# Optimization experiments

Measured on AMD Instinct MI355X. Metric: run time of the kernel, lower is better.

The kernel has to match this reference:

```python
import jax, jax.numpy as jnp
import numpy as np

EPS = 1e-6      # vector-neuron epsilon
BN_EPS = 1e-5   # torch BatchNorm eps
NEG = 0.2       # LeakyReLU negative slope
K = 20


def knn_idx(flat, k):
    # flat: [B, D, N] flattened (C*3) features; returns kNN indices [B, N, k]
    xx = jnp.sum(flat * flat, axis=1)                     # [B, N]
    inner = jnp.einsum('bdn,bdm->bnm', flat, flat)        # [B, N, N]
    neg_dist = 2.0 * inner - xx[:, :, None] - xx[:, None, :]
    return jax.lax.top_k(neg_dist, k)[1]                  # [B, N, k]


def graph_feature(x, k):
    # x: [B, C, 3, N] -> [B, 2C, 3, N, k] = cat(neighbor - center, center)
    B, C, _, N = x.shape
    idx = knn_idx(x.reshape(B, C * 3, N), k)              # [B, N, k]
    xt = jnp.transpose(x, (0, 3, 1, 2))                   # [B, N, C, 3]
    nbr = jax.vmap(lambda f, i: f[i])(xt, idx)            # [B, N, k, C, 3]
    ctr = jnp.broadcast_to(xt[:, :, None], nbr.shape)
    feat = jnp.concatenate([nbr - ctr, ctr], axis=3)      # [B, N, k, 2C, 3]
    return jnp.transpose(feat, (0, 3, 4, 1, 2))


def vn_bn(x, w, b):
    # VNBatchNorm (training-mode batch stats): normalize the per-vector norm.
    # x: [B, C, 3, ...]
    norm = jnp.sqrt(jnp.sum(x * x, axis=2)) + EPS         # [B, C, ...]
    axes = (0,) + tuple(range(2, norm.ndim))
    mean = jnp.mean(norm, axis=axes, keepdims=True)
    var = jnp.mean((norm - mean) ** 2, axis=axes, keepdims=True)
    shp = (1, -1) + (1,) * (norm.ndim - 2)
    nbn = (norm - mean) / jnp.sqrt(var + BN_EPS) * w.reshape(shp) + b.reshape(shp)
    return x * jnp.expand_dims(nbn / norm, 2)


def vn_lrelu(x, wf, wd, bnw, bnb):
    # VNLinearLeakyReLU: linear over channel dim, VN batchnorm, directional LeakyReLU
    p = jnp.einsum('oi,bi...->bo...', wf, x)
    p = vn_bn(p, bnw, bnb)
    d = jnp.einsum('oi,bi...->bo...', wd, x)
    dot = jnp.sum(p * d, axis=2, keepdims=True)
    dsq = jnp.sum(d * d, axis=2, keepdims=True)
    mask = (dot >= 0).astype(x.dtype)
    return NEG * p + (1.0 - NEG) * (mask * p + (1.0 - mask) * (p - (dot / (dsq + EPS)) * d))


def setup_inputs() -> dict:
    key = jax.random.key(0)
    ks = jax.random.split(key, 12)
    H, C = 64, 128
    lin = lambda k, o, i: jax.random.normal(k, (o, i), jnp.float32) / np.sqrt(i)
    return {
        'x': jax.random.normal(ks[0], (8, 1024, 3), jnp.float32),
        'w1f': lin(ks[1], H, 2), 'w1d': lin(ks[2], H, 2),
        'bn1w': jnp.ones(H), 'bn1b': jnp.zeros(H),
        'w2f': lin(ks[3], H, 2 * H), 'w2d': lin(ks[4], H, 2 * H),
        'bn2w': jnp.ones(H), 'bn2b': jnp.zeros(H),
        'w3f': lin(ks[5], H, 2 * H), 'w3d': lin(ks[6], H, 2 * H),
        'bn3w': jnp.ones(H), 'bn3b': jnp.zeros(H),
        'w4f': lin(ks[7], H, 2 * H), 'w4d': lin(ks[8], H, 2 * H),
        'bn4w': jnp.ones(H), 'bn4b': jnp.zeros(H),
        'wcf': lin(ks[9], C, 4 * H), 'wcd': lin(ks[10], 1, 4 * H),
        'bncw': jnp.ones(C), 'bncb': jnp.zeros(C),
    }


def reference(x, w1f, w1d, bn1w, bn1b, w2f, w2d, bn2w, bn2b,
              w3f, w3d, bn3w, bn3b, w4f, w4d, bn4w, bn4b,
              wcf, wcd, bncw, bncb):
    pts = jnp.transpose(x, (0, 2, 1))[:, None]            # [B, 1, 3, N]
    h = vn_lrelu(graph_feature(pts, K), w1f, w1d, bn1w, bn1b)
    x1 = jnp.mean(h, axis=-1)                             # [B, H, 3, N]
    h = vn_lrelu(graph_feature(x1, K), w2f, w2d, bn2w, bn2b)
    x2 = jnp.mean(h, axis=-1)
    h = vn_lrelu(graph_feature(x2, K), w3f, w3d, bn3w, bn3b)
    x3 = jnp.mean(h, axis=-1)
    h = vn_lrelu(graph_feature(x3, K), w4f, w4d, bn4w, bn4b)
    x4 = jnp.mean(h, axis=-1)
    cat = jnp.concatenate([x1, x2, x3, x4], axis=1)       # [B, 4H, 3, N]
    out = vn_lrelu(cat, wcf, wcd, bncw, bncb)             # [B, c_dim, 3, N]
    return jnp.mean(out, axis=-1)                         # [B, c_dim, 3]
```

## Files before the change

kernel.cpp:

```cpp
#include <hip/hip_runtime.h>

#define NPTS 1024
#define NB 8
#define KNN 20
#define N3 (3*NPTS)
#define CHT 256
#define BSX (CHT*N3)

constexpr int OFF_X0    = 0;
constexpr int OFF_XFEAT = OFF_X0 + NB*N3;
constexpr int OFF_YAP   = OFF_XFEAT + NB*CHT*N3;
constexpr int OFF_YBP   = OFF_YAP + NB*N3*64;
constexpr int OFF_YAD   = OFF_YBP + NB*N3*64;
constexpr int OFF_YBD   = OFF_YAD + NB*N3*64;
constexpr int OFF_XX    = OFF_YBD + NB*N3*64;
constexpr int OFF_WCFT  = OFF_XX + NB*NPTS;
constexpr int OFF_STATS = OFF_WCFT + 256*128;
constexpr int OFF_IDX   = OFF_STATS + 5*256;
constexpr int OFF_PF    = OFF_YAP;
constexpr int OFF_DF    = OFF_YAD;

__global__ void k_transpose(const float* __restrict__ x, float* __restrict__ x0) {
  int t = blockIdx.x*256 + threadIdx.x;
  int b = t >> 10, n = t & 1023;
  const float* p = x + t*3;
  x0[b*N3 + n]          = p[0];
  x0[b*N3 + NPTS + n]   = p[1];
  x0[b*N3 + 2*NPTS + n] = p[2];
}

__global__ __launch_bounds__(256) void k_xx2(const float* __restrict__ Fb, int bs, int D,
                                             float* __restrict__ xx) {
  __shared__ float sm[4][64];
  int tid = threadIdx.x;
  int p = tid & 63, g = tid >> 6;
  int t = blockIdx.x * 64 + p;
  int b = t >> 10, m = t & 1023;
  int s = (D * g) >> 2, e = (D * (g + 1)) >> 2;
  const float* f = Fb + b*bs + m;
  float a = 0.f;
  for (int d = s; d < e; ++d) { float v = f[d*NPTS]; a = fmaf(v, v, a); }
  sm[g][p] = a;
  __syncthreads();
  if (g == 0) xx[t] = ((sm[0][p] + sm[1][p]) + sm[2][p]) + sm[3][p];
}

__global__ __launch_bounds__(512) void k_knn2(const float* __restrict__ Fb, int bs, int D,
                                              const float* __restrict__ xx,
                                              int* __restrict__ idxo) {
  __shared__ float xs[8][NPTS];
  int g  = blockIdx.x;
  int wg = (g & 7)*64 + (g >> 3);
  int b  = wg >> 6;
  int n0 = (wg & 63) << 4;
  int tid = threadIdx.x;
  int w = tid >> 6, lane = tid & 63;
  const float* f = Fb + b*bs;

  int row0 = n0 + 2*w, row1 = row0 + 1;
  float acc0[16], acc1[16];
  #pragma unroll
  for (int s = 0; s < 16; ++s) { acc0[s] = 0.f; acc1[s] = 0.f; }

  int nt = (D + 7) >> 3;
  for (int t = 0; t < nt; ++t) {
    int d0 = t << 3;
    int cnt = D - d0; if (cnt > 8) cnt = 8;
    __syncthreads();
    #pragma unroll
    for (int u = 0; u < 4; ++u) {
      int e = tid + (u << 9);
      int dd = e >> 8, mq = (e & 255) << 2;
      if (dd < cnt)
        *(float4*)&xs[dd][mq] = *(const float4*)&f[(d0 + dd)*NPTS + mq];
    }
    __syncthreads();
    for (int dd = 0; dd < cnt; ++dd) {
      float rf0 = xs[dd][row0];
      float rf1 = xs[dd][row1];
      #pragma unroll
      for (int s2 = 0; s2 < 4; ++s2) {
        float4 xm = *(const float4*)&xs[dd][(lane << 2) + (s2 << 8)];
        acc0[s2*4+0] = fmaf(rf0, xm.x, acc0[s2*4+0]);
        acc0[s2*4+1] = fmaf(rf0, xm.y, acc0[s2*4+1]);
        acc0[s2*4+2] = fmaf(rf0, xm.z, acc0[s2*4+2]);
        acc0[s2*4+3] = fmaf(rf0, xm.w, acc0[s2*4+3]);
        acc1[s2*4+0] = fmaf(rf1, xm.x, acc1[s2*4+0]);
        acc1[s2*4+1] = fmaf(rf1, xm.y, acc1[s2*4+1]);
        acc1[s2*4+2] = fmaf(rf1, xm.z, acc1[s2*4+2]);
        acc1[s2*4+3] = fmaf(rf1, xm.w, acc1[s2*4+3]);
      }
    }
  }

  unsigned ord0[16], ord1[16];
  float xxr0 = xx[b*NPTS + row0];
  float xxr1 = xx[b*NPTS + row1];
  #pragma unroll
  for (int s2 = 0; s2 < 4; ++s2) {
    float4 xv = *(const float4*)&xx[b*NPTS + (lane << 2) + (s2 << 8)];
    float xm4[4] = {xv.x, xv.y, xv.z, xv.w};
    #pragma unroll
    for (int q = 0; q < 4; ++q) {
      int s = s2*4 + q;
      float v0 = (2.f*acc0[s] - xxr0) - xm4[q];
      float v1 = (2.f*acc1[s] - xxr1) - xm4[q];
      unsigned u0 = __float_as_uint(v0);
      unsigned u1 = __float_as_uint(v1);
      ord0[s] = (u0 & 0x80000000u) ? ~u0 : (u0 | 0x80000000u);
      ord1[s] = (u1 & 0x80000000u) ? ~u1 : (u1 | 0x80000000u);
    }
  }

  unsigned base4L = (unsigned)(lane << 2);
  unsigned cl0 = 0xFFFFFFFFu, cl1 = 0xFFFFFFFFu;
  int winm0 = 0, winm1 = 0;
  for (int it = 0; it < KNN; ++it) {
    unsigned bo0 = 0u, bc0 = 0u, bo1 = 0u, bc1 = 0u;
    #pragma unroll
    for (int s = 0; s < 16; ++s) {
      const unsigned Cs = (unsigned)(((s >> 2) << 8) | (s & 3));
      unsigned v0 = ord0[s]; v0 = (cl0 == Cs) ? 0u : v0; ord0[s] = v0;
      if (v0 > bo0) { bo0 = v0; bc0 = Cs; }
      unsigned v1 = ord1[s]; v1 = (cl1 == Cs) ? 0u : v1; ord1[s] = v1;
      if (v1 > bo1) { bo1 = v1; bc1 = Cs; }
    }
    unsigned m0 = base4L + bc0, m1 = base4L + bc1;
    unsigned long long K0 = ((unsigned long long)bo0 << 32) | (unsigned long long)(1023u - m0);
    unsigned long long K1 = ((unsigned long long)bo1 << 32) | (unsigned long long)(1023u - m1);
    unsigned long long myK0 = K0, myK1 = K1;
    #pragma unroll
    for (int off = 1; off < 64; off <<= 1) {
      unsigned long long o0 = __shfl_xor(K0, off, 64);
      unsigned long long o1 = __shfl_xor(K1, off, 64);
      K0 = (o0 > K0) ? o0 : K0;
      K1 = (o1 > K1) ? o1 : K1;
    }
    cl0 = (K0 == myK0) ? bc0 : 0xFFFFFFFFu;
    cl1 = (K1 == myK1) ? bc1 : 0xFFFFFFFFu;
    if (lane == it) {
      winm0 = 1023 - (int)(unsigned)(K0 & 0xFFFFFFFFull);
      winm1 = 1023 - (int)(unsigned)(K1 & 0xFFFFFFFFull);
    }
  }
  if (lane < KNN) {
    idxo[(b*NPTS + row0)*KNN + lane] = winm0;
    idxo[(b*NPTS + row1)*KNN + lane] = winm1;
  }
}

template<int DIN>
__global__ __launch_bounds__(256) void k_linear3(const float* __restrict__ xin, int bsx,
                                                 const float* __restrict__ w,
                                                 float* __restrict__ yA, float* __restrict__ yB) {
  __shared__ float wA[DIN*64], wB[DIN*64];
  int tid = threadIdx.x;
  for (int e = tid; e < 64*DIN; e += 256) {
    int o = e & 63, i = e >> 6;
    float a = w[o*(2*DIN) + i];
    wA[i*64 + o] = a;
    wB[i*64 + o] = w[o*(2*DIN) + DIN + i] - a;
  }
  __syncthreads();
  int o = tid & 63, ns = tid >> 6;
  int b = blockIdx.y / 3, v = blockIdx.y % 3;
  int n0 = blockIdx.x * 64 + ns * 16;
  const float* xb = xin + b*bsx + v*NPTS + n0;
  float ap[16], bp[16];
  #pragma unroll
  for (int j = 0; j < 16; ++j) { ap[j] = 0.f; bp[j] = 0.f; }
  for (int i = 0; i < DIN; ++i) {
    float wa = wA[i*64 + o], wb = wB[i*64 + o];
    #pragma unroll
    for (int q = 0; q < 4; ++q) {
      float4 xv = *(const float4*)&xb[i*N3 + q*4];
      ap[q*4+0] = fmaf(wa, xv.x, ap[q*4+0]); bp[q*4+0] = fmaf(wb, xv.x, bp[q*4+0]);
      ap[q*4+1] = fmaf(wa, xv.y, ap[q*4+1]); bp[q*4+1] = fmaf(wb, xv.y, bp[q*4+1]);
      ap[q*4+2] = fmaf(wa, xv.z, ap[q*4+2]); bp[q*4+2] = fmaf(wb, xv.z, bp[q*4+2]);
      ap[q*4+3] = fmaf(wa, xv.w, ap[q*4+3]); bp[q*4+3] = fmaf(wb, xv.w, bp[q*4+3]);
    }
  }
  int base = ((b*3 + v)*NPTS + n0)*64 + o;
  #pragma unroll
  for (int j = 0; j < 16; ++j) { yA[base + j*64] = ap[j]; yB[base + j*64] = bp[j]; }
}

__global__ __launch_bounds__(256) void k_stats2(const float* __restrict__ yAp, const float* __restrict__ yBp,
                                                const int* __restrict__ idxo, float* __restrict__ statsL) {
  __shared__ float rs[256], rss[256];
  int tid = threadIdx.x; int o = tid & 63, w = tid >> 6;
  int blk = blockIdx.x;
  int wg = ((blk & 7) << 8) | (blk >> 3);
  int b = wg >> 8;
  int n = ((wg & 255) << 2) + w;
  float s = 0.f, ss = 0.f;
  int i0 = (b*3*NPTS + n)*64 + o;
  float c0 = yBp[i0], c1 = yBp[i0 + NPTS*64], c2 = yBp[i0 + 2*NPTS*64];
  const int* ir = idxo + (b*NPTS + n)*KNN;
  for (int kk = 0; kk < KNN; ++kk) {
    int m = ir[kk];
    int gg = (b*3*NPTS + m)*64 + o;
    float p0 = yAp[gg] + c0;
    float p1 = yAp[gg + NPTS*64] + c1;
    float p2 = yAp[gg + 2*NPTS*64] + c2;
    float nrm = sqrtf(p0*p0 + p1*p1 + p2*p2) + 1e-6f;
    s += nrm; ss = fmaf(nrm, nrm, ss);
  }
  rs[tid] = s; rss[tid] = ss;
  __syncthreads();
  if (tid < 64) {
    float a  = rs[tid]  + rs[tid+64]  + rs[tid+128]  + rs[tid+192];
    float as = rss[tid] + rss[tid+64] + rss[tid+128] + rss[tid+192];
    atomicAdd(&statsL[tid], a);
    atomicAdd(&statsL[128 + tid], as);
  }
}

__global__ __launch_bounds__(256) void k_apply(const float* __restrict__ yAp, const float* __restrict__ yBp,
                                               const float* __restrict__ yAd, const float* __restrict__ yBd,
                                               const int* __restrict__ idxo, const float* __restrict__ statsL,
                                               const float* __restrict__ bnw, const float* __restrict__ bnb,
                                               float* __restrict__ xfeat, int coff) {
  int tid = threadIdx.x; int o = tid & 63, w = tid >> 6;
  int blk = blockIdx.x;
  int wg = ((blk & 7) << 8) | (blk >> 3);
  int b = wg >> 8;
  int n = ((wg & 255) << 2) + w;
  const float cntInv = 1.f / 163840.f;
  float mean = statsL[o] * cntInv;
  float var  = statsL[128 + o] * cntInv - mean*mean;
  float istd = rsqrtf(var + 1e-5f);
  float wN = bnw[o], bN = bnb[o];
  int i0 = (b*3*NPTS + n)*64 + o;
  float cp0 = yBp[i0], cp1 = yBp[i0 + NPTS*64], cp2 = yBp[i0 + 2*NPTS*64];
  float cd0 = yBd[i0], cd1 = yBd[i0 + NPTS*64], cd2 = yBd[i0 + 2*NPTS*64];
  const int* ir = idxo + (b*NPTS + n)*KNN;
  float a0 = 0.f, a1 = 0.f, a2 = 0.f;
  for (int kk = 0; kk < KNN; ++kk) {
    int m = ir[kk];
    int gg = (b*3*NPTS + m)*64 + o;
    float p0 = yAp[gg] + cp0, p1 = yAp[gg + NPTS*64] + cp1, p2 = yAp[gg + 2*NPTS*64] + cp2;
    float d0 = yAd[gg] + cd0, d1 = yAd[gg + NPTS*64] + cd1, d2 = yAd[gg + 2*NPTS*64] + cd2;
    float nrm = sqrtf(p0*p0 + p1*p1 + p2*p2) + 1e-6f;
    float sc = ((nrm - mean)*istd*wN + bN) / nrm;
    p0 *= sc; p1 *= sc; p2 *= sc;
    float dot = p0*d0 + p1*d1 + p2*d2;
    float dsq = d0*d0 + d1*d1 + d2*d2;
    float coef = (dot < 0.f) ? (0.8f * dot / (dsq + 1e-6f)) : 0.f;
    a0 += p0 - coef*d0; a1 += p1 - coef*d1; a2 += p2 - coef*d2;
  }
  int ob = ((b*CHT + coff + o)*3)*NPTS + n;
  xfeat[ob]          = a0 * 0.05f;
  xfeat[ob + NPTS]   = a1 * 0.05f;
  xfeat[ob + 2*NPTS] = a2 * 0.05f;
}

__global__ void k_wcfT(const float* __restrict__ wcf, float* __restrict__ wT) {
  int e = blockIdx.x*256 + threadIdx.x;
  int o = e >> 8, i = e & 255;
  wT[i*128 + o] = wcf[e];
}

__global__ __launch_bounds__(256) void k_pF3(const float* __restrict__ xfeat, const float* __restrict__ wT,
                                             const float* __restrict__ wcd,
                                             float* __restrict__ pF, float* __restrict__ dF) {
  __shared__ float xs[256][32];
  __shared__ float dpart[8][32];
  int tid = threadIdx.x;
  int b = blockIdx.y / 3, v = blockIdx.y % 3;
  int n0 = blockIdx.x * 32;
  const float* xb = xfeat + b*BSX + v*NPTS + n0;
  #pragma unroll
  for (int u = 0; u < 8; ++u) {
    int e = tid + (u << 8);
    int i = e >> 3, sl = (e & 7) << 2;
    *(float4*)&xs[i][sl] = *(const float4*)&xb[i*N3 + sl];
  }
  __syncthreads();
  int o = tid & 127, h = tid >> 7;
  float a[16];
  #pragma unroll
  for (int j = 0; j < 16; ++j) a[j] = 0.f;
  for (int i = 0; i < 256; ++i) {
    float wv = wT[i*128 + o];
    #pragma unroll
    for (int q = 0; q < 4; ++q) {
      float4 xv = *(const float4*)&xs[i][h*16 + q*4];
      a[q*4+0] = fmaf(wv, xv.x, a[q*4+0]);
      a[q*4+1] = fmaf(wv, xv.y, a[q*4+1]);
      a[q*4+2] = fmaf(wv, xv.z, a[q*4+2]);
      a[q*4+3] = fmaf(wv, xv.w, a[q*4+3]);
    }
  }
  int base = ((b*3 + v)*NPTS + n0 + h*16)*128 + o;
  #pragma unroll
  for (int j = 0; j < 16; ++j) pF[base + j*128] = a[j];
  int nn = tid & 31, gI = tid >> 5;
  float dp = 0.f;
  for (int i = gI*32; i < gI*32 + 32; ++i) dp = fmaf(wcd[i], xs[i][nn], dp);
  dpart[gI][nn] = dp;
  __syncthreads();
  if (tid < 32) {
    float aa = 0.f;
    #pragma unroll
    for (int gq = 0; gq < 8; ++gq) aa += dpart[gq][tid];
    dF[(b*3 + v)*NPTS + n0 + tid] = aa;
  }
}

__global__ __launch_bounds__(256) void k_statsF2(const float* __restrict__ pF, float* __restrict__ statsF) {
  int tid = threadIdx.x; int o = tid & 127, half = tid >> 7;
  int blk = blockIdx.x;
  int b = blk >> 6, n0 = (blk & 63) << 4;
  float s = 0.f, ss = 0.f;
  for (int j = 0; j < 8; ++j) {
    int n = n0 + half + (j << 1);
    int g = (b*3*NPTS + n)*128 + o;
    float p0 = pF[g], p1 = pF[g + NPTS*128], p2 = pF[g + 2*NPTS*128];
    float nrm = sqrtf(p0*p0 + p1*p1 + p2*p2) + 1e-6f;
    s += nrm; ss = fmaf(nrm, nrm, ss);
  }
  atomicAdd(&statsF[o], s);
  atomicAdd(&statsF[128 + o], ss);
}

__global__ __launch_bounds__(256) void k_final2(const float* __restrict__ pF, const float* __restrict__ dF,
                                                const float* __restrict__ statsF,
                                                const float* __restrict__ bncw, const float* __restrict__ bncb,
                                                float* __restrict__ out) {
  int tid = threadIdx.x; int o = tid & 127, half = tid >> 7;
  int blk = blockIdx.x;
  int b = blk >> 5, n0 = (blk & 31) << 5;
  const float cntInv = 1.f / 8192.f;
  float mean = statsF[o] * cntInv;
  float var  = statsF[128 + o] * cntInv - mean*mean;
  float istd = rsqrtf(var + 1e-5f);
  float wN = bncw[o], bN = bncb[o];
  float a0 = 0.f, a1 = 0.f, a2 = 0.f;
  for (int j = 0; j < 16; ++j) {
    int n = n0 + half + (j << 1);
    int g = (b*3*NPTS + n)*128 + o;
    float p0 = pF[g], p1 = pF[g + NPTS*128], p2 = pF[g + 2*NPTS*128];
    int dg = b*N3 + n;
    float d0 = dF[dg], d1 = dF[dg + NPTS], d2 = dF[dg + 2*NPTS];
    float nrm = sqrtf(p0*p0 + p1*p1 + p2*p2) + 1e-6f;
    float sc = ((nrm - mean)*istd*wN + bN) / nrm;
    p0 *= sc; p1 *= sc; p2 *= sc;
    float dot = p0*d0 + p1*d1 + p2*d2;
    float dsq = d0*d0 + d1*d1 + d2*d2;
    float coef = (dot < 0.f) ? (0.8f * dot / (dsq + 1e-6f)) : 0.f;
    a0 += p0 - coef*d0; a1 += p1 - coef*d1; a2 += p2 - coef*d2;
  }
  float scl = 1.f / 1024.f;
  int ob = (b*128 + o)*3;
  atomicAdd(&out[ob],     a0*scl);
  atomicAdd(&out[ob + 1], a1*scl);
  atomicAdd(&out[ob + 2], a2*scl);
}

extern "C" void kernel_launch(void* const* d_in, const int* in_sizes, int n_in,
                              void* d_out, int out_size, void* d_ws, size_t ws_size,
                              hipStream_t stream) {
  (void)in_sizes; (void)n_in; (void)ws_size;
  const float* x = (const float*)d_in[0];
  const float* wF[4]  = {(const float*)d_in[1],  (const float*)d_in[5],
                         (const float*)d_in[9],  (const float*)d_in[13]};
  const float* wD[4]  = {(const float*)d_in[2],  (const float*)d_in[6],
                         (const float*)d_in[10], (const float*)d_in[14]};
  const float* bnW[4] = {(const float*)d_in[3],  (const float*)d_in[7],
                         (const float*)d_in[11], (const float*)d_in[15]};
  const float* bnB[4] = {(const float*)d_in[4],  (const float*)d_in[8],
                         (const float*)d_in[12], (const float*)d_in[16]};
  const float* wcf  = (const float*)d_in[17];
  const float* wcd  = (const float*)d_in[18];
  const float* bncw = (const float*)d_in[19];
  const float* bncb = (const float*)d_in[20];

  float* ws    = (float*)d_ws;
  float* x0    = ws + OFF_X0;
  float* xfeat = ws + OFF_XFEAT;
  float* yAp   = ws + OFF_YAP;
  float* yBp   = ws + OFF_YBP;
  float* yAd   = ws + OFF_YAD;
  float* yBd   = ws + OFF_YBD;
  float* pF    = ws + OFF_PF;
  float* dF    = ws + OFF_DF;
  float* xx    = ws + OFF_XX;
  float* wT    = ws + OFF_WCFT;
  float* stats = ws + OFF_STATS;
  int*   idx   = (int*)(ws + OFF_IDX);

  hipMemsetAsync(stats, 0, 5*256*sizeof(float), stream);
  hipMemsetAsync(d_out, 0, (size_t)out_size*sizeof(float), stream);

  k_transpose<<<NB*NPTS/256, 256, 0, stream>>>(x, x0);
  k_wcfT<<<128, 256, 0, stream>>>(wcf, wT);

  for (int L = 0; L < 4; ++L) {
    const float* fin = (L == 0) ? x0 : (xfeat + (L-1)*64*N3);
    int bs = (L == 0) ? N3 : BSX;
    int D  = (L == 0) ? 3 : 192;
    k_xx2<<<NB*NPTS/64, 256, 0, stream>>>(fin, bs, D, xx);
    k_knn2<<<512, 512, 0, stream>>>(fin, bs, D, xx, idx);
    if (L == 0) {
      k_linear3<1><<<dim3(16, 24), 256, 0, stream>>>(fin, bs, wF[0], yAp, yBp);
      k_linear3<1><<<dim3(16, 24), 256, 0, stream>>>(fin, bs, wD[0], yAd, yBd);
    } else {
      k_linear3<64><<<dim3(16, 24), 256, 0, stream>>>(fin, bs, wF[L], yAp, yBp);
      k_linear3<64><<<dim3(16, 24), 256, 0, stream>>>(fin, bs, wD[L], yAd, yBd);
    }
    k_stats2<<<2048, 256, 0, stream>>>(yAp, yBp, idx, stats + L*256);
    k_apply<<<2048, 256, 0, stream>>>(yAp, yBp, yAd, yBd, idx, stats + L*256,
                                      bnW[L], bnB[L], xfeat, L*64);
  }

  k_pF3<<<dim3(32, 24), 256, 0, stream>>>(xfeat, wT, wcd, pF, dF);
  k_statsF2<<<512, 256, 0, stream>>>(pF, stats + 4*256);
  k_final2<<<256, 256, 0, stream>>>(pF, dF, stats + 4*256, bncw, bncb, (float*)d_out);
}
```

Before: 1.020 ms.

## Fuse prep kernels, double-buffer kNN with in-kernel norms, merge linear passes

```diff
diff --git a/kernel.cpp b/kernel.cpp
--- a/kernel.cpp
+++ b/kernel.cpp
@@ -13,176 +13,267 @@
 constexpr int OFF_YBP   = OFF_YAP + NB*N3*64;
 constexpr int OFF_YAD   = OFF_YBP + NB*N3*64;
 constexpr int OFF_YBD   = OFF_YAD + NB*N3*64;
-constexpr int OFF_XX    = OFF_YBD + NB*N3*64;
-constexpr int OFF_WCFT  = OFF_XX + NB*NPTS;
+constexpr int OFF_WCFT  = OFF_YBD + NB*N3*64;
 constexpr int OFF_STATS = OFF_WCFT + 256*128;
 constexpr int OFF_IDX   = OFF_STATS + 5*256;
+constexpr int OFF_W4    = OFF_IDX + NB*NPTS*KNN;
 constexpr int OFF_PF    = OFF_YAP;
 constexpr int OFF_DF    = OFF_YAD;
 
-__global__ void k_transpose(const float* __restrict__ x, float* __restrict__ x0) {
-  int t = blockIdx.x*256 + threadIdx.x;
-  int b = t >> 10, n = t & 1023;
-  const float* p = x + t*3;
-  x0[b*N3 + n]          = p[0];
-  x0[b*N3 + NPTS + n]   = p[1];
-  x0[b*N3 + 2*NPTS + n] = p[2];
-}
-
-__global__ __launch_bounds__(256) void k_xx2(const float* __restrict__ Fb, int bs, int D,
-                                             float* __restrict__ xx) {
-  __shared__ float sm[4][64];
-  int tid = threadIdx.x;
-  int p = tid & 63, g = tid >> 6;
-  int t = blockIdx.x * 64 + p;
-  int b = t >> 10, m = t & 1023;
-  int s = (D * g) >> 2, e = (D * (g + 1)) >> 2;
-  const float* f = Fb + b*bs + m;
-  float a = 0.f;
-  for (int d = s; d < e; ++d) { float v = f[d*NPTS]; a = fmaf(v, v, a); }
-  sm[g][p] = a;
-  __syncthreads();
-  if (g == 0) xx[t] = ((sm[0][p] + sm[1][p]) + sm[2][p]) + sm[3][p];
-}
-
-__global__ __launch_bounds__(512) void k_knn2(const float* __restrict__ Fb, int bs, int D,
-                                              const float* __restrict__ xx,
+__global__ __launch_bounds__(256) void k_prep(
+    const float* __restrict__ x,
+    const float* __restrict__ w1f, const float* __restrict__ w1d,
+    const float* __restrict__ w2f, const float* __restrict__ w2d,
+    const float* __restrict__ w3f, const float* __restrict__ w3d,
+    const float* __restrict__ w4f, const float* __restrict__ w4d,
+    const float* __restrict__ wcf,
+    float* __restrict__ x0, float* __restrict__ w4, float* __restrict__ wT) {
+  int blk = blockIdx.x, tid = threadIdx.x;
+  if (blk < 32) {
+    int t = blk*256 + tid;
+    int b = t >> 10, n = t & 1023;
+    const float* p = x + t*3;
+    x0[b*N3 + n]          = p[0];
+    x0[b*N3 + NPTS + n]   = p[1];
+    x0[b*N3 + 2*NPTS + n] = p[2];
+  } else if (blk == 32) {
+    if (tid < 64) {
+      int o = tid;
+      float a0 = w1f[o*2], a1 = w1f[o*2+1];
+      float d0 = w1d[o*2], d1 = w1d[o*2+1];
+      float* dst = w4 + o*4;
+      dst[0] = a0; dst[1] = a1 - a0; dst[2] = d0; dst[3] = d1 - d0;
+    }
+  } else if (blk < 36) {
+    int L = blk - 32;
+    const float* wf = (L == 1) ? w2f : (L == 2) ? w3f : w4f;
+    const float* wd = (L == 1) ? w2d : (L == 2) ? w3d : w4d;
+    float* dst = w4 + L*16384;
+    for (int u = 0; u < 64; ++u) {
+      int e = tid + u*256;
+      int i = e >> 8, oc = e & 255, o = oc >> 2, c = oc & 3;
+      float v;
+      if (c == 0)      v = wf[o*128 + i];
+      else if (c == 1) v = wf[o*128 + 64 + i] - wf[o*128 + i];
+      else if (c == 2) v = wd[o*128 + i];
+      else             v = wd[o*128 + 64 + i] - wd[o*128 + i];
+      dst[e] = v;
+    }
+  } else {
+    int e0 = (blk - 36) * 8192;
+    for (int u = 0; u < 32; ++u) {
+      int e = e0 + tid + u*256;
+      int o = e >> 8, i = e & 255;
+      wT[i*128 + o] = wcf[e];
+    }
+  }
+}
+
+__global__ __launch_bounds__(512) void k_knn3(const float* __restrict__ Fb, int bs, int D,
                                               int* __restrict__ idxo) {
-  __shared__ float xs[8][NPTS];
+  __shared__ float xs[2][8][NPTS];
   int g  = blockIdx.x;
-  int wg = (g & 7)*64 + (g >> 3);
-  int b  = wg >> 6;
-  int n0 = (wg & 63) << 4;
+  int wg = (g & 7)*32 + (g >> 3);
+  int b  = wg >> 5;
+  int n0 = (wg & 31) << 5;
   int tid = threadIdx.x;
   int w = tid >> 6, lane = tid & 63;
-  const float* f = Fb + b*bs;
-
-  int row0 = n0 + 2*w, row1 = row0 + 1;
-  float acc0[16], acc1[16];
-  #pragma unroll
-  for (int s = 0; s < 16; ++s) { acc0[s] = 0.f; acc1[s] = 0.f; }
+  int rowbase = n0 + (w << 2);
+  const float* f = Fb + (size_t)b*bs;
+
+  float acc[4][16], xxm[16], xxr[4];
+  #pragma unroll
+  for (int r = 0; r < 4; ++r) xxr[r] = 0.f;
+  #pragma unroll
+  for (int s = 0; s < 16; ++s) {
+    xxm[s] = 0.f;
+    #pragma unroll
+    for (int r = 0; r < 4; ++r) acc[r][s] = 0.f;
+  }
+
+  int cnt0 = (D < 8) ? D : 8;
+  #pragma unroll
+  for (int u = 0; u < 4; ++u) {
+    int e = tid + (u << 9);
+    int dd = e >> 8, mq = (e & 255) << 2;
+    if (dd < cnt0)
+      *(float4*)&xs[0][dd][mq] = *(const float4*)&f[(size_t)dd*NPTS + mq];
+  }
+  __syncthreads();
 
   int nt = (D + 7) >> 3;
   for (int t = 0; t < nt; ++t) {
-    int d0 = t << 3;
-    int cnt = D - d0; if (cnt > 8) cnt = 8;
+    int cur = t & 1;
+    int cnt = D - (t << 3); if (cnt > 8) cnt = 8;
+    float4 pf[4];
+    if (t + 1 < nt) {
+      int d0 = (t + 1) << 3;
+      #pragma unroll
+      for (int u = 0; u < 4; ++u) {
+        int e = tid + (u << 9);
+        int dd = e >> 8, mq = (e & 255) << 2;
+        pf[u] = *(const float4*)&f[(size_t)(d0 + dd)*NPTS + mq];
+      }
+    }
+    if (cnt == 8) {
+      #pragma unroll
+      for (int dd = 0; dd < 8; ++dd) {
+        float4 rf = *(const float4*)&xs[cur][dd][rowbase];
+        xxr[0] = fmaf(rf.x, rf.x, xxr[0]);
+        xxr[1] = fmaf(rf.y, rf.y, xxr[1]);
+        xxr[2] = fmaf(rf.z, rf.z, xxr[2]);
+        xxr[3] = fmaf(rf.w, rf.w, xxr[3]);
+        #pragma unroll
+        for (int s2 = 0; s2 < 4; ++s2) {
+          float4 xm = *(const float4*)&xs[cur][dd][(lane << 2) + (s2 << 8)];
+          float xm4[4] = {xm.x, xm.y, xm.z, xm.w};
+          #pragma unroll
+          for (int q = 0; q < 4; ++q) {
+            int s = s2*4 + q;
+            xxm[s] = fmaf(xm4[q], xm4[q], xxm[s]);
+            acc[0][s] = fmaf(rf.x, xm4[q], acc[0][s]);
+            acc[1][s] = fmaf(rf.y, xm4[q], acc[1][s]);
+            acc[2][s] = fmaf(rf.z, xm4[q], acc[2][s]);
+            acc[3][s] = fmaf(rf.w, xm4[q], acc[3][s]);
+          }
+        }
+      }
+    } else {
+      for (int dd = 0; dd < cnt; ++dd) {
+        float4 rf = *(const float4*)&xs[cur][dd][rowbase];
+        xxr[0] = fmaf(rf.x, rf.x, xxr[0]);
+        xxr[1] = fmaf(rf.y, rf.y, xxr[1]);
+        xxr[2] = fmaf(rf.z, rf.z, xxr[2]);
+        xxr[3] = fmaf(rf.w, rf.w, xxr[3]);
+        #pragma unroll
+        for (int s2 = 0; s2 < 4; ++s2) {
+          float4 xm = *(const float4*)&xs[cur][dd][(lane << 2) + (s2 << 8)];
+          float xm4[4] = {xm.x, xm.y, xm.z, xm.w};
+          #pragma unroll
+          for (int q = 0; q < 4; ++q) {
+            int s = s2*4 + q;
+            xxm[s] = fmaf(xm4[q], xm4[q], xxm[s]);
+            acc[0][s] = fmaf(rf.x, xm4[q], acc[0][s]);
+            acc[1][s] = fmaf(rf.y, xm4[q], acc[1][s]);
+            acc[2][s] = fmaf(rf.z, xm4[q], acc[2][s]);
+            acc[3][s] = fmaf(rf.w, xm4[q], acc[3][s]);
+          }
+        }
+      }
+    }
+    if (t + 1 < nt) {
+      int nb = cur ^ 1;
+      #pragma unroll
+      for (int u = 0; u < 4; ++u) {
+        int e = tid + (u << 9);
+        int dd = e >> 8, mq = (e & 255) << 2;
+        *(float4*)&xs[nb][dd][mq] = pf[u];
+      }
+    }
     __syncthreads();
+  }
+
+  #pragma unroll
+  for (int r = 0; r < 4; ++r)
     #pragma unroll
-    for (int u = 0; u < 4; ++u) {
-      int e = tid + (u << 9);
-      int dd = e >> 8, mq = (e & 255) << 2;
-      if (dd < cnt)
-        *(float4*)&xs[dd][mq] = *(const float4*)&f[(d0 + dd)*NPTS + mq];
-    }
-    __syncthreads();
-    for (int dd = 0; dd < cnt; ++dd) {
-      float rf0 = xs[dd][row0];
-      float rf1 = xs[dd][row1];
+    for (int s = 0; s < 16; ++s)
+      acc[r][s] = (2.f*acc[r][s] - xxr[r]) - xxm[s];
+
+  const float NEGINF = -3.402823466e38f;
+  #pragma unroll
+  for (int pr = 0; pr < 2; ++pr) {
+    const int rA = pr*2, rB = pr*2 + 1;
+    unsigned clA = 0xFFFFu, clB = 0xFFFFu;
+    int winA = 0, winB = 0;
+    for (int it = 0; it < KNN; ++it) {
+      float boA = NEGINF, boB = NEGINF;
+      unsigned bcA = 0u, bcB = 0u;
       #pragma unroll
-      for (int s2 = 0; s2 < 4; ++s2) {
-        float4 xm = *(const float4*)&xs[dd][(lane << 2) + (s2 << 8)];
-        acc0[s2*4+0] = fmaf(rf0, xm.x, acc0[s2*4+0]);
-        acc0[s2*4+1] = fmaf(rf0, xm.y, acc0[s2*4+1]);
-        acc0[s2*4+2] = fmaf(rf0, xm.z, acc0[s2*4+2]);
-        acc0[s2*4+3] = fmaf(rf0, xm.w, acc0[s2*4+3]);
-        acc1[s2*4+0] = fmaf(rf1, xm.x, acc1[s2*4+0]);
-        acc1[s2*4+1] = fmaf(rf1, xm.y, acc1[s2*4+1]);
-        acc1[s2*4+2] = fmaf(rf1, xm.z, acc1[s2*4+2]);
-        acc1[s2*4+3] = fmaf(rf1, xm.w, acc1[s2*4+3]);
-      }
-    }
-  }
-
-  unsigned ord0[16], ord1[16];
-  float xxr0 = xx[b*NPTS + row0];
-  float xxr1 = xx[b*NPTS + row1];
-  #pragma unroll
-  for (int s2 = 0; s2 < 4; ++s2) {
-    float4 xv = *(const float4*)&xx[b*NPTS + (lane << 2) + (s2 << 8)];
-    float xm4[4] = {xv.x, xv.y, xv.z, xv.w};
-    #pragma unroll
-    for (int q = 0; q < 4; ++q) {
-      int s = s2*4 + q;
-      float v0 = (2.f*acc0[s] - xxr0) - xm4[q];
-      float v1 = (2.f*acc1[s] - xxr1) - xm4[q];
-      unsigned u0 = __float_as_uint(v0);
-      unsigned u1 = __float_as_uint(v1);
-      ord0[s] = (u0 & 0x80000000u) ? ~u0 : (u0 | 0x80000000u);
-      ord1[s] = (u1 & 0x80000000u) ? ~u1 : (u1 | 0x80000000u);
-    }
-  }
-
-  unsigned base4L = (unsigned)(lane << 2);
-  unsigned cl0 = 0xFFFFFFFFu, cl1 = 0xFFFFFFFFu;
-  int winm0 = 0, winm1 = 0;
-  for (int it = 0; it < KNN; ++it) {
-    unsigned bo0 = 0u, bc0 = 0u, bo1 = 0u, bc1 = 0u;
-    #pragma unroll
-    for (int s = 0; s < 16; ++s) {
-      const unsigned Cs = (unsigned)(((s >> 2) << 8) | (s & 3));
-      unsigned v0 = ord0[s]; v0 = (cl0 == Cs) ? 0u : v0; ord0[s] = v0;
-      if (v0 > bo0) { bo0 = v0; bc0 = Cs; }
-      unsigned v1 = ord1[s]; v1 = (cl1 == Cs) ? 0u : v1; ord1[s] = v1;
-      if (v1 > bo1) { bo1 = v1; bc1 = Cs; }
-    }
-    unsigned m0 = base4L + bc0, m1 = base4L + bc1;
-    unsigned long long K0 = ((unsigned long long)bo0 << 32) | (unsigned long long)(1023u - m0);
-    unsigned long long K1 = ((unsigned long long)bo1 << 32) | (unsigned long long)(1023u - m1);
-    unsigned long long myK0 = K0, myK1 = K1;
-    #pragma unroll
-    for (int off = 1; off < 64; off <<= 1) {
-      unsigned long long o0 = __shfl_xor(K0, off, 64);
-      unsigned long long o1 = __shfl_xor(K1, off, 64);
-      K0 = (o0 > K0) ? o0 : K0;
-      K1 = (o1 > K1) ? o1 : K1;
-    }
-    cl0 = (K0 == myK0) ? bc0 : 0xFFFFFFFFu;
-    cl1 = (K1 == myK1) ? bc1 : 0xFFFFFFFFu;
-    if (lane == it) {
-      winm0 = 1023 - (int)(unsigned)(K0 & 0xFFFFFFFFull);
-      winm1 = 1023 - (int)(unsigned)(K1 & 0xFFFFFFFFull);
-    }
-  }
-  if (lane < KNN) {
-    idxo[(b*NPTS + row0)*KNN + lane] = winm0;
-    idxo[(b*NPTS + row1)*KNN + lane] = winm1;
-  }
-}
-
-template<int DIN>
-__global__ __launch_bounds__(256) void k_linear3(const float* __restrict__ xin, int bsx,
-                                                 const float* __restrict__ w,
-                                                 float* __restrict__ yA, float* __restrict__ yB) {
-  __shared__ float wA[DIN*64], wB[DIN*64];
+      for (int s = 0; s < 16; ++s) {
+        const unsigned Cs = (unsigned)(((s >> 2) << 8) | (s & 3));
+        float vA = acc[rA][s]; vA = (clA == Cs) ? NEGINF : vA; acc[rA][s] = vA;
+        if (vA > boA) { boA = vA; bcA = Cs; }
+        float vB = acc[rB][s]; vB = (clB == Cs) ? NEGINF : vB; acc[rB][s] = vB;
+        if (vB > boB) { boB = vB; bcB = Cs; }
+      }
+      int mA = (lane << 2) | (int)(bcA & 3u) | (int)(bcA & 0x300u);
+      int mB = (lane << 2) | (int)(bcB & 3u) | (int)(bcB & 0x300u);
+      float wmA = boA, wmB = boB;
+      #pragma unroll
+      for (int off = 1; off < 64; off <<= 1) {
+        float tA = __shfl_xor(wmA, off, 64);
+        float tB = __shfl_xor(wmB, off, 64);
+        wmA = fmaxf(wmA, tA);
+        wmB = fmaxf(wmB, tB);
+      }
+      unsigned long long balA = __ballot(boA == wmA);
+      int win_mA;
+      if (__popcll(balA) == 1) {
+        int wl = __ffsll((long long)balA) - 1;
+        win_mA = __shfl(mA, wl, 64);
+      } else {
+        int cA = (boA == wmA) ? (1023 - mA) : -1;
+        #pragma unroll
+        for (int off = 1; off < 64; off <<= 1) { int tc = __shfl_xor(cA, off, 64); cA = max(cA, tc); }
+        win_mA = 1023 - cA;
+      }
+      clA = (boA == wmA && mA == win_mA) ? bcA : 0xFFFFu;
+      if (lane == it) winA = win_mA;
+      unsigned long long balB = __ballot(boB == wmB);
+      int win_mB;
+      if (__popcll(balB) == 1) {
+        int wl = __ffsll((long long)balB) - 1;
+        win_mB = __shfl(mB, wl, 64);
+      } else {
+        int cB = (boB == wmB) ? (1023 - mB) : -1;
+        #pragma unroll
+        for (int off = 1; off < 64; off <<= 1) { int tc = __shfl_xor(cB, off, 64); cB = max(cB, tc); }
+        win_mB = 1023 - cB;
+      }
+      clB = (boB == wmB && mB == win_mB) ? bcB : 0xFFFFu;
+      if (lane == it) winB = win_mB;
+    }
+    if (lane < KNN) {
+      idxo[(b*NPTS + rowbase + rA)*KNN + lane] = winA;
+      idxo[(b*NPTS + rowbase + rB)*KNN + lane] = winB;
+    }
+  }
+}
+
+__global__ __launch_bounds__(256) void k_linear4(const float* __restrict__ xin, int bsx,
+                                                 const float* __restrict__ w4, int DIN,
+                                                 float* __restrict__ yAp, float* __restrict__ yBp,
+                                                 float* __restrict__ yAd, float* __restrict__ yBd) {
   int tid = threadIdx.x;
-  for (int e = tid; e < 64*DIN; e += 256) {
-    int o = e & 63, i = e >> 6;
-    float a = w[o*(2*DIN) + i];
-    wA[i*64 + o] = a;
-    wB[i*64 + o] = w[o*(2*DIN) + DIN + i] - a;
-  }
-  __syncthreads();
   int o = tid & 63, ns = tid >> 6;
   int b = blockIdx.y / 3, v = blockIdx.y % 3;
-  int n0 = blockIdx.x * 64 + ns * 16;
-  const float* xb = xin + b*bsx + v*NPTS + n0;
-  float ap[16], bp[16];
-  #pragma unroll
-  for (int j = 0; j < 16; ++j) { ap[j] = 0.f; bp[j] = 0.f; }
+  int n0 = blockIdx.x * 32 + ns * 8;
+  const float* xb = xin + (size_t)b*bsx + v*NPTS + n0;
+  float aF[8], bF[8], aD[8], bD[8];
+  #pragma unroll
+  for (int j = 0; j < 8; ++j) { aF[j] = 0.f; bF[j] = 0.f; aD[j] = 0.f; bD[j] = 0.f; }
+  #pragma unroll 4
   for (int i = 0; i < DIN; ++i) {
-    float wa = wA[i*64 + o], wb = wB[i*64 + o];
+    float4 wv  = *(const float4*)&w4[(i << 8) + (o << 2)];
+    float4 xlo = *(const float4*)&xb[i*N3];
+    float4 xhi = *(const float4*)&xb[i*N3 + 4];
+    float xv[8] = {xlo.x, xlo.y, xlo.z, xlo.w, xhi.x, xhi.y, xhi.z, xhi.w};
     #pragma unroll
-    for (int q = 0; q < 4; ++q) {
-      float4 xv = *(const float4*)&xb[i*N3 + q*4];
-      ap[q*4+0] = fmaf(wa, xv.x, ap[q*4+0]); bp[q*4+0] = fmaf(wb, xv.x, bp[q*4+0]);
-      ap[q*4+1] = fmaf(wa, xv.y, ap[q*4+1]); bp[q*4+1] = fmaf(wb, xv.y, bp[q*4+1]);
-      ap[q*4+2] = fmaf(wa, xv.z, ap[q*4+2]); bp[q*4+2] = fmaf(wb, xv.z, bp[q*4+2]);
-      ap[q*4+3] = fmaf(wa, xv.w, ap[q*4+3]); bp[q*4+3] = fmaf(wb, xv.w, bp[q*4+3]);
+    for (int j = 0; j < 8; ++j) {
+      aF[j] = fmaf(wv.x, xv[j], aF[j]);
+      bF[j] = fmaf(wv.y, xv[j], bF[j]);
+      aD[j] = fmaf(wv.z, xv[j], aD[j]);
+      bD[j] = fmaf(wv.w, xv[j], bD[j]);
     }
   }
   int base = ((b*3 + v)*NPTS + n0)*64 + o;
   #pragma unroll
-  for (int j = 0; j < 16; ++j) { yA[base + j*64] = ap[j]; yB[base + j*64] = bp[j]; }
+  for (int j = 0; j < 8; ++j) {
+    yAp[base + j*64] = aF[j];
+    yBp[base + j*64] = bF[j];
+    yAd[base + j*64] = aD[j];
+    yBd[base + j*64] = bD[j];
+  }
 }
 
 __global__ __launch_bounds__(256) void k_stats2(const float* __restrict__ yAp, const float* __restrict__ yBp,
@@ -193,12 +284,19 @@
   int wg = ((blk & 7) << 8) | (blk >> 3);
   int b = wg >> 8;
   int n = ((wg & 255) << 2) + w;
-  float s = 0.f, ss = 0.f;
+  const int* ir = idxo + (b*NPTS + n)*KNN;
+  int4 ir0 = *(const int4*)&ir[0],  ir1 = *(const int4*)&ir[4];
+  int4 ir2 = *(const int4*)&ir[8],  ir3 = *(const int4*)&ir[12];
+  int4 ir4 = *(const int4*)&ir[16];
+  int mm[20] = {ir0.x,ir0.y,ir0.z,ir0.w, ir1.x,ir1.y,ir1.z,ir1.w,
+                ir2.x,ir2.y,ir2.z,ir2.w, ir3.x,ir3.y,ir3.z,ir3.w,
+                ir4.x,ir4.y,ir4.z,ir4.w};
   int i0 = (b*3*NPTS + n)*64 + o;
   float c0 = yBp[i0], c1 = yBp[i0 + NPTS*64], c2 = yBp[i0 + 2*NPTS*64];
-  const int* ir = idxo + (b*NPTS + n)*KNN;
+  float s = 0.f, ss = 0.f;
+  #pragma unroll
   for (int kk = 0; kk < KNN; ++kk) {
-    int m = ir[kk];
+    int m = mm[kk];
     int gg = (b*3*NPTS + m)*64 + o;
     float p0 = yAp[gg] + c0;
     float p1 = yAp[gg + NPTS*64] + c1;
@@ -235,9 +333,16 @@
   float cp0 = yBp[i0], cp1 = yBp[i0 + NPTS*64], cp2 = yBp[i0 + 2*NPTS*64];
   float cd0 = yBd[i0], cd1 = yBd[i0 + NPTS*64], cd2 = yBd[i0 + 2*NPTS*64];
   const int* ir = idxo + (b*NPTS + n)*KNN;
+  int4 ir0 = *(const int4*)&ir[0],  ir1 = *(const int4*)&ir[4];
+  int4 ir2 = *(const int4*)&ir[8],  ir3 = *(const int4*)&ir[12];
+  int4 ir4 = *(const int4*)&ir[16];
+  int mm[20] = {ir0.x,ir0.y,ir0.z,ir0.w, ir1.x,ir1.y,ir1.z,ir1.w,
+                ir2.x,ir2.y,ir2.z,ir2.w, ir3.x,ir3.y,ir3.z,ir3.w,
+                ir4.x,ir4.y,ir4.z,ir4.w};
   float a0 = 0.f, a1 = 0.f, a2 = 0.f;
+  #pragma unroll
   for (int kk = 0; kk < KNN; ++kk) {
-    int m = ir[kk];
+    int m = mm[kk];
     int gg = (b*3*NPTS + m)*64 + o;
     float p0 = yAp[gg] + cp0, p1 = yAp[gg + NPTS*64] + cp1, p2 = yAp[gg + 2*NPTS*64] + cp2;
     float d0 = yAd[gg] + cd0, d1 = yAd[gg + NPTS*64] + cd1, d2 = yAd[gg + 2*NPTS*64] + cd2;
@@ -255,12 +360,6 @@
   xfeat[ob + 2*NPTS] = a2 * 0.05f;
 }
 
-__global__ void k_wcfT(const float* __restrict__ wcf, float* __restrict__ wT) {
-  int e = blockIdx.x*256 + threadIdx.x;
-  int o = e >> 8, i = e & 255;
-  wT[i*128 + o] = wcf[e];
-}
-
 __global__ __launch_bounds__(256) void k_pF3(const float* __restrict__ xfeat, const float* __restrict__ wT,
                                              const float* __restrict__ wcd,
                                              float* __restrict__ pF, float* __restrict__ dF) {
@@ -269,7 +368,7 @@
   int tid = threadIdx.x;
   int b = blockIdx.y / 3, v = blockIdx.y % 3;
   int n0 = blockIdx.x * 32;
-  const float* xb = xfeat + b*BSX + v*NPTS + n0;
+  const float* xb = xfeat + (size_t)b*BSX + v*NPTS + n0;
   #pragma unroll
   for (int u = 0; u < 8; ++u) {
     int e = tid + (u << 8);
@@ -363,10 +462,6 @@
                               hipStream_t stream) {
   (void)in_sizes; (void)n_in; (void)ws_size;
   const float* x = (const float*)d_in[0];
-  const float* wF[4]  = {(const float*)d_in[1],  (const float*)d_in[5],
-                         (const float*)d_in[9],  (const float*)d_in[13]};
-  const float* wD[4]  = {(const float*)d_in[2],  (const float*)d_in[6],
-                         (const float*)d_in[10], (const float*)d_in[14]};
   const float* bnW[4] = {(const float*)d_in[3],  (const float*)d_in[7],
                          (const float*)d_in[11], (const float*)d_in[15]};
   const float* bnB[4] = {(const float*)d_in[4],  (const float*)d_in[8],
@@ -385,30 +480,29 @@
   float* yBd   = ws + OFF_YBD;
   float* pF    = ws + OFF_PF;
   float* dF    = ws + OFF_DF;
-  float* xx    = ws + OFF_XX;
   float* wT    = ws + OFF_WCFT;
   float* stats = ws + OFF_STATS;
   int*   idx   = (int*)(ws + OFF_IDX);
+  float* w4    = ws + OFF_W4;
 
   hipMemsetAsync(stats, 0, 5*256*sizeof(float), stream);
   hipMemsetAsync(d_out, 0, (size_t)out_size*sizeof(float), stream);
 
-  k_transpose<<<NB*NPTS/256, 256, 0, stream>>>(x, x0);
-  k_wcfT<<<128, 256, 0, stream>>>(wcf, wT);
+  k_prep<<<40, 256, 0, stream>>>(x,
+      (const float*)d_in[1], (const float*)d_in[2],
+      (const float*)d_in[5], (const float*)d_in[6],
+      (const float*)d_in[9], (const float*)d_in[10],
+      (const float*)d_in[13], (const float*)d_in[14],
+      wcf, x0, w4, wT);
 
   for (int L = 0; L < 4; ++L) {
     const float* fin = (L == 0) ? x0 : (xfeat + (L-1)*64*N3);
     int bs = (L == 0) ? N3 : BSX;
     int D  = (L == 0) ? 3 : 192;
-    k_xx2<<<NB*NPTS/64, 256, 0, stream>>>(fin, bs, D, xx);
-    k_knn2<<<512, 512, 0, stream>>>(fin, bs, D, xx, idx);
-    if (L == 0) {
-      k_linear3<1><<<dim3(16, 24), 256, 0, stream>>>(fin, bs, wF[0], yAp, yBp);
-      k_linear3<1><<<dim3(16, 24), 256, 0, stream>>>(fin, bs, wD[0], yAd, yBd);
-    } else {
-      k_linear3<64><<<dim3(16, 24), 256, 0, stream>>>(fin, bs, wF[L], yAp, yBp);
-      k_linear3<64><<<dim3(16, 24), 256, 0, stream>>>(fin, bs, wD[L], yAd, yBd);
-    }
+    int DIN = (L == 0) ? 1 : 64;
+    k_knn3<<<256, 512, 0, stream>>>(fin, bs, D, idx);
+    k_linear4<<<dim3(32, 24), 256, 0, stream>>>(fin, bs, w4 + L*16384, DIN,
+                                                yAp, yBp, yAd, yBd);
     k_stats2<<<2048, 256, 0, stream>>>(yAp, yBp, idx, stats + L*256);
     k_apply<<<2048, 256, 0, stream>>>(yAp, yBp, yAd, yBd, idx, stats + L*256,
                                       bnW[L], bnB[L], xfeat, L*64);
```

After: 1.034 ms. Within noise of the previous version (+1.4%).
